# Performance work log

Hardware: AMD Instinct MI355X
Metric: run time of the kernel (lower is better)

The kernel has to match this reference:

```python
import jax, jax.numpy as jnp
import numpy as np

N = 100000   # nodes
E = 800000   # edges
IN = 128     # in_channels == embedding_size (required by residual Linear)
EMB = 128
OUT = 64
EPS = 1e-5   # GraphNorm eps (PyG default)


def setup_inputs() -> dict:
    key = jax.random.key(0)
    ks = jax.random.split(key, 8)
    x = jax.random.normal(ks[0], (N, IN), jnp.float32)
    edge_index = jax.random.randint(ks[1], (2, E), 0, N, dtype=jnp.int64)
    g = lambda k, shape, scale: jax.random.normal(k, shape, jnp.float32) * scale
    return dict(
        x=x,
        edge_index=edge_index,
        W1=g(ks[2], (IN, EMB), IN ** -0.5), b1=jnp.zeros((EMB,), jnp.float32),
        W2=g(ks[3], (EMB, EMB), EMB ** -0.5), b2=jnp.zeros((EMB,), jnp.float32),
        gn1_w=1.0 + g(ks[4], (EMB,), 0.05), gn1_b=jnp.zeros((EMB,), jnp.float32), gn1_ms=jnp.ones((EMB,), jnp.float32),
        gn2_w=1.0 + g(ks[5], (EMB,), 0.05), gn2_b=jnp.zeros((EMB,), jnp.float32), gn2_ms=jnp.ones((EMB,), jnp.float32),
        Wr=g(ks[6], (EMB, OUT), EMB ** -0.5), br=jnp.zeros((OUT,), jnp.float32),
    )


def _gcn_conv(x, W, b, src, dst, dinv):
    # PyG GCNConv: h = x @ W; out[i] = sum_{(j->i)} dinv[j]*dinv[i]*h[j]; out += bias
    h = x @ W
    norm = (dinv[src] * dinv[dst])[:, None]        # [E+N, 1]
    msg = h[src] * norm                             # gather + scale (irregular)
    out = jax.ops.segment_sum(msg, dst, num_segments=N)  # scatter-add
    return out + b


def _graph_norm(h, w, b, ms):
    # PyG GraphNorm, single graph: mean/var over node dim
    mean = jnp.mean(h, axis=0)
    c = h - ms * mean
    var = jnp.mean(c * c, axis=0)
    return w * c * jax.lax.rsqrt(var + EPS) + b


def reference(x, edge_index, W1, b1, W2, b2, gn1_w, gn1_b, gn1_ms, gn2_w, gn2_b, gn2_ms, Wr, br):
    loops = jnp.arange(N, dtype=edge_index.dtype)
    src = jnp.concatenate([edge_index[0], loops])   # add self-loops
    dst = jnp.concatenate([edge_index[1], loops])
    deg = jax.ops.segment_sum(jnp.ones_like(src, dtype=x.dtype), dst, num_segments=N)
    dinv = jnp.where(deg > 0, jax.lax.rsqrt(jnp.maximum(deg, 1.0)), 0.0)

    # dropout is identity in eval mode
    x1 = jax.nn.relu(_graph_norm(_gcn_conv(x, W1, b1, src, dst, dinv), gn1_w, gn1_b, gn1_ms))
    x2 = jax.nn.relu(_graph_norm(_gcn_conv(x1, W2, b2, src, dst, dinv), gn2_w, gn2_b, gn2_ms))
    return (x1 + x2) @ Wr + br
```

## Files before the change

### kernel.cpp

```cpp
#include <hip/hip_runtime.h>
#include <hip/hip_bf16.h>

typedef __attribute__((ext_vector_type(8))) short bf16x8;
typedef __attribute__((ext_vector_type(4))) float f32x4;

#define STATS_BLOCKS 512
#define SLOTS 32

__device__ __forceinline__ float bf2f(unsigned short u){
  union { unsigned int i; float f; } v; v.i = ((unsigned int)u) << 16; return v.f;
}
__device__ __forceinline__ unsigned short f2bf(float f){
  union { float f; unsigned int i; } v; v.f = f;
  return (unsigned short)((v.i + 0x7fffu + ((v.i >> 16) & 1u)) >> 16);
}


__global__ __launch_bounds__(256) void k_zero(int* cur, int N){
  int i = blockIdx.x*256 + threadIdx.x;
  if (i < N) cur[i] = 0;
}

__global__ __launch_bounds__(256) void k_build(const int* __restrict__ src,
    const int* __restrict__ dst, int* cur, int* col, int E){
  int e = blockIdx.x*256 + threadIdx.x;
  if (e >= E) return;
  int d = dst[e];
  int s = src[e];
  int p = atomicAdd(&cur[d], 1);
  if (p < SLOTS) col[d*SLOTS + p] = s;
}

__global__ __launch_bounds__(256) void k_dinv(const int* __restrict__ cur,
                                              float* dinv, int* cnt, int N){
  int i = blockIdx.x*256 + threadIdx.x;
  if (i < N){
    int c = cur[i];
    dinv[i] = rsqrtf((float)(1 + c));
    cnt[i] = min(c, SLOTS);
  }
}


__global__ __launch_bounds__(256) void k_pack(const float* __restrict__ W,
                                              unsigned short* __restrict__ wp, int ncols){
  int idx = blockIdx.x*256 + threadIdx.x;
  if (idx >= 128*ncols) return;
  int b = idx & 7, lane = (idx>>3)&63, kk = (idx>>9)&3, ct = idx>>11;
  int k = kk*32 + ((lane>>4)<<3) + b;
  int c = ct*16 + (lane&15);
  wp[idx] = f2bf(W[k*ncols + c]);
}


__global__ __launch_bounds__(256) void k_gemm1(const float* __restrict__ A,
    const unsigned short* __restrict__ wp, const float* __restrict__ dinv,
    unsigned short* __restrict__ h, int nTiles){
  int gw = (int)((blockIdx.x*256 + threadIdx.x) >> 6);
  if (gw >= nTiles) return;
  int lane = threadIdx.x & 63;
  int row0 = gw*16;
  int r  = row0 + (lane & 15);
  int kb = (lane >> 4) * 8;
  bf16x8 a[4];
#pragma unroll
  for (int kk = 0; kk < 4; ++kk){
    const float* p = A + (size_t)r*128 + kk*32 + kb;
    f32x4 v0 = *reinterpret_cast<const f32x4*>(p);
    f32x4 v1 = *reinterpret_cast<const f32x4*>(p + 4);
#pragma unroll
    for (int b = 0; b < 4; ++b){ a[kk][b] = (short)f2bf(v0[b]); a[kk][4+b] = (short)f2bf(v1[b]); }
  }
  int cst = lane & 15;
  int rb  = row0 + ((lane >> 4) << 2);
  float dv[4];
#pragma unroll
  for (int b2 = 0; b2 < 4; ++b2) dv[b2] = dinv[rb + b2];
#pragma unroll
  for (int ct = 0; ct < 8; ++ct){
    f32x4 acc = {0.f,0.f,0.f,0.f};
#pragma unroll
    for (int kk = 0; kk < 4; ++kk){
      bf16x8 b = *reinterpret_cast<const bf16x8*>(wp + ((ct*4 + kk)*64 + lane)*8);
      acc = __builtin_amdgcn_mfma_f32_16x16x32_bf16(a[kk], b, acc, 0, 0, 0);
    }
    int c = ct*16 + cst;
#pragma unroll
    for (int b2 = 0; b2 < 4; ++b2)
      h[(size_t)(rb + b2)*128 + c] = f2bf(dv[b2]*acc[b2]);
  }
}


__global__ __launch_bounds__(256) void k_agg(const unsigned short* __restrict__ h,
    const float* __restrict__ dinv, const int* __restrict__ cnt,
    const int* __restrict__ col, const float* __restrict__ bias,
    unsigned short* __restrict__ agg, int N){
  int i = (int)((blockIdx.x*256 + threadIdx.x) >> 6);
  if (i >= N) return;
  int lane = threadIdx.x & 63;
  int q  = lane >> 4;
  int cl = lane & 15;
  int c = cnt[i];
  int idx = (lane < c) ? col[i*SLOTS + lane] : i;
  int m16 = (c + 15) & ~15;
  int pads = m16 - c;
  float acc[8];
#pragma unroll
  for (int b = 0; b < 8; ++b) acc[b] = 0.f;
  for (int j = 0; j < m16; j += 16){
    int r0 = __shfl(idx, j + q);
    int r1 = __shfl(idx, j + 4 + q);
    int r2 = __shfl(idx, j + 8 + q);
    int r3 = __shfl(idx, j + 12 + q);
    bf16x8 v0 = *reinterpret_cast<const bf16x8*>(h + (size_t)r0*128 + cl*8);
    bf16x8 v1 = *reinterpret_cast<const bf16x8*>(h + (size_t)r1*128 + cl*8);
    bf16x8 v2 = *reinterpret_cast<const bf16x8*>(h + (size_t)r2*128 + cl*8);
    bf16x8 v3 = *reinterpret_cast<const bf16x8*>(h + (size_t)r3*128 + cl*8);
#pragma unroll
    for (int b = 0; b < 8; ++b)
      acc[b] += (bf2f((unsigned short)v0[b]) + bf2f((unsigned short)v1[b]))
              + (bf2f((unsigned short)v2[b]) + bf2f((unsigned short)v3[b]));
  }
#pragma unroll
  for (int b = 0; b < 8; ++b){
    acc[b] += __shfl_xor(acc[b], 16);
    acc[b] += __shfl_xor(acc[b], 32);
  }
  if (q == 0){
    bf16x8 hs = *reinterpret_cast<const bf16x8*>(h + (size_t)i*128 + cl*8);
    float di = dinv[i];
    float fm = (float)(pads - 1);
    bf16x8 o;
#pragma unroll
    for (int b = 0; b < 8; ++b){
      float s = bf2f((unsigned short)hs[b]);
      float v = di*(acc[b] - fm*s) + bias[cl*8 + b];
      o[b] = (short)f2bf(v);
    }
    *reinterpret_cast<bf16x8*>(agg + (size_t)i*128 + cl*8) = o;
  }
}


__global__ __launch_bounds__(256) void k_stats(const unsigned short* __restrict__ agg,
    float* __restrict__ partials, int N){
  int tid = blockIdx.x*256 + threadIdx.x;
  int g = threadIdx.x & 15;
  int c0 = g * 8;
  float S1[8] = {0,0,0,0,0,0,0,0}, S2[8] = {0,0,0,0,0,0,0,0};
  size_t total = (size_t)N * 16;
  for (size_t p = tid; p < total; p += (size_t)STATS_BLOCKS*256){
    bf16x8 v = reinterpret_cast<const bf16x8*>(agg)[p];
#pragma unroll
    for (int b = 0; b < 8; ++b){
      float f = bf2f((unsigned short)v[b]);
      S1[b] += f; S2[b] += f*f;
    }
  }
  __shared__ float sh1[16][128];
  __shared__ float sh2[16][128];
  int cp = threadIdx.x >> 4;
#pragma unroll
  for (int b = 0; b < 8; ++b){ sh1[cp][c0 + b] = S1[b]; sh2[cp][c0 + b] = S2[b]; }
  __syncthreads();
  int t = threadIdx.x;
  if (t < 128){
    float s = 0.f;
#pragma unroll
    for (int qq = 0; qq < 16; ++qq) s += sh1[qq][t];
    partials[blockIdx.x*256 + t] = s;
  } else {
    int cc = t - 128;
    float s = 0.f;
#pragma unroll
    for (int qq = 0; qq < 16; ++qq) s += sh2[qq][cc];
    partials[blockIdx.x*256 + 128 + cc] = s;
  }
}


__global__ void k_reduce(const float* __restrict__ partials, const float* __restrict__ gw_,
    const float* __restrict__ gb_, const float* __restrict__ gms_,
    float* __restrict__ st, int N){
  int c = threadIdx.x;
  if (c >= 128) return;
  float S1 = 0.f, S2 = 0.f;
  for (int b = 0; b < STATS_BLOCKS; ++b){
    S1 += partials[b*256 + c];
    S2 += partials[b*256 + 128 + c];
  }
  float m  = S1 / (float)N;
  float ms = gms_[c];
  float var = S2/(float)N - 2.f*ms*m*m + ms*ms*m*m;
  float rs = rsqrtf(var + 1e-5f);
  float wv = gw_[c];
  st[c]       = wv * rs;
  st[128 + c] = gb_[c] - wv*rs*ms*m;
}


__global__ __launch_bounds__(256) void k_gemm2(const unsigned short* __restrict__ agg,
    const float* __restrict__ st, const unsigned short* __restrict__ wp,
    const float* __restrict__ dinv, unsigned short* __restrict__ h, int nTiles){
  int gw = (int)((blockIdx.x*256 + threadIdx.x) >> 6);
  if (gw >= nTiles) return;
  int lane = threadIdx.x & 63;
  int row0 = gw*16;
  int r  = row0 + (lane & 15);
  int kb = (lane >> 4) * 8;
  bf16x8 a[4];
#pragma unroll
  for (int kk = 0; kk < 4; ++kk){
    int cb = kk*32 + kb;
    bf16x8 v = *reinterpret_cast<const bf16x8*>(agg + (size_t)r*128 + cb);
    f32x4 s0 = *reinterpret_cast<const f32x4*>(st + cb);
    f32x4 s1 = *reinterpret_cast<const f32x4*>(st + cb + 4);
    f32x4 t0 = *reinterpret_cast<const f32x4*>(st + 128 + cb);
    f32x4 t1 = *reinterpret_cast<const f32x4*>(st + 128 + cb + 4);
#pragma unroll
    for (int b = 0; b < 4; ++b){
      a[kk][b]   = (short)f2bf(fmaxf(0.f, s0[b]*bf2f((unsigned short)v[b])   + t0[b]));
      a[kk][4+b] = (short)f2bf(fmaxf(0.f, s1[b]*bf2f((unsigned short)v[4+b]) + t1[b]));
    }
  }
  int cst = lane & 15;
  int rb  = row0 + ((lane >> 4) << 2);
  float dv[4];
#pragma unroll
  for (int b2 = 0; b2 < 4; ++b2) dv[b2] = dinv[rb + b2];
#pragma unroll
  for (int ct = 0; ct < 8; ++ct){
    f32x4 acc = {0.f,0.f,0.f,0.f};
#pragma unroll
    for (int kk = 0; kk < 4; ++kk){
      bf16x8 b = *reinterpret_cast<const bf16x8*>(wp + ((ct*4 + kk)*64 + lane)*8);
      acc = __builtin_amdgcn_mfma_f32_16x16x32_bf16(a[kk], b, acc, 0, 0, 0);
    }
    int c = ct*16 + cst;
#pragma unroll
    for (int b2 = 0; b2 < 4; ++b2)
      h[(size_t)(rb + b2)*128 + c] = f2bf(dv[b2]*acc[b2]);
  }
}


__global__ __launch_bounds__(256) void k_final(const unsigned short* __restrict__ agg1,
    const unsigned short* __restrict__ agg2, const float* __restrict__ st,
    const unsigned short* __restrict__ wp, const float* __restrict__ br,
    float* __restrict__ out, int nTiles){
  int gw = (int)((blockIdx.x*256 + threadIdx.x) >> 6);
  if (gw >= nTiles) return;
  int lane = threadIdx.x & 63;
  int row0 = gw*16;
  int r  = row0 + (lane & 15);
  int kb = (lane >> 4) * 8;
  bf16x8 a[4];
#pragma unroll
  for (int kk = 0; kk < 4; ++kk){
    int cb = kk*32 + kb;
    bf16x8 g1 = *reinterpret_cast<const bf16x8*>(agg1 + (size_t)r*128 + cb);
    bf16x8 g2 = *reinterpret_cast<const bf16x8*>(agg2 + (size_t)r*128 + cb);
#pragma unroll
    for (int b = 0; b < 8; ++b){
      int c = cb + b;
      float x1v = bf2f(f2bf(fmaxf(0.f, st[c]*bf2f((unsigned short)g1[b]) + st[128 + c])));
      float r2  = fmaxf(0.f, st[256 + c]*bf2f((unsigned short)g2[b]) + st[384 + c]);
      a[kk][b] = (short)f2bf(x1v + r2);
    }
  }
  int cst = lane & 15;
  int rb  = row0 + ((lane >> 4) << 2);
#pragma unroll
  for (int ct = 0; ct < 4; ++ct){
    f32x4 acc = {0.f,0.f,0.f,0.f};
#pragma unroll
    for (int kk = 0; kk < 4; ++kk){
      bf16x8 b = *reinterpret_cast<const bf16x8*>(wp + ((ct*4 + kk)*64 + lane)*8);
      acc = __builtin_amdgcn_mfma_f32_16x16x32_bf16(a[kk], b, acc, 0, 0, 0);
    }
    int c = ct*16 + cst;
    float bias = br[c];
#pragma unroll
    for (int b2 = 0; b2 < 4; ++b2)
      out[(size_t)(rb + b2)*64 + c] = acc[b2] + bias;
  }
}


extern "C" void kernel_launch(void* const* d_in, const int* in_sizes, int n_in,
                              void* d_out, int out_size, void* d_ws, size_t ws_size,
                              hipStream_t stream){
  const float* x    = (const float*)d_in[0];
  const int*   ei   = (const int*)d_in[1];
  const float* W1   = (const float*)d_in[2];
  const float* b1   = (const float*)d_in[3];
  const float* W2   = (const float*)d_in[4];
  const float* b2   = (const float*)d_in[5];
  const float* g1w  = (const float*)d_in[6];
  const float* g1b  = (const float*)d_in[7];
  const float* g1ms = (const float*)d_in[8];
  const float* g2w  = (const float*)d_in[9];
  const float* g2b  = (const float*)d_in[10];
  const float* g2ms = (const float*)d_in[11];
  const float* Wr   = (const float*)d_in[12];
  const float* br   = (const float*)d_in[13];
  float* out = (float*)d_out;

  int N = in_sizes[0] / 128;
  int E = in_sizes[1] / 2;
  const int* srcp = ei;
  const int* dstp = ei + E;

  char* w = (char*)d_ws;
  auto alloc = [&](size_t bytes){ char* p = w; w += (bytes + 255) & ~(size_t)255; return p; };
  float* dinv          = (float*)alloc((size_t)N*4);
  int*   cur           = (int*)  alloc((size_t)N*4);
  int*   cnt           = (int*)  alloc((size_t)N*4);
  int*   col           = (int*)  alloc((size_t)N*SLOTS*4);
  float* partials      = (float*)alloc((size_t)STATS_BLOCKS*256*4);
  float* st            = (float*)alloc(4*128*4);
  unsigned short* wp1  = (unsigned short*)alloc(128*128*2);
  unsigned short* wp2  = (unsigned short*)alloc(128*128*2);
  unsigned short* wpr  = (unsigned short*)alloc(128*64*2);
  unsigned short* h    = (unsigned short*)alloc((size_t)N*128*2);
  unsigned short* agg1 = (unsigned short*)alloc((size_t)N*128*2);
  unsigned short* agg2 = (unsigned short*)alloc((size_t)N*128*2);

  int nTiles = N / 16;
  int gemmBlocks = (nTiles + 3) / 4;
  int nB = (N + 255)/256, eB = (E + 255)/256;
  int aggBlocks = (N*64 + 255)/256;

  k_zero <<<nB, 256, 0, stream>>>(cur, N);
  k_build<<<eB, 256, 0, stream>>>(srcp, dstp, cur, col, E);
  k_dinv <<<nB, 256, 0, stream>>>(cur, dinv, cnt, N);

  k_pack<<<(128*128 + 255)/256, 256, 0, stream>>>(W1, wp1, 128);
  k_pack<<<(128*128 + 255)/256, 256, 0, stream>>>(W2, wp2, 128);
  k_pack<<<(128*64  + 255)/256, 256, 0, stream>>>(Wr, wpr, 64);

  k_gemm1<<<gemmBlocks, 256, 0, stream>>>(x, wp1, dinv, h, nTiles);
  k_agg  <<<aggBlocks, 256, 0, stream>>>(h, dinv, cnt, col, b1, agg1, N);
  k_stats<<<STATS_BLOCKS, 256, 0, stream>>>(agg1, partials, N);
  k_reduce<<<1, 128, 0, stream>>>(partials, g1w, g1b, g1ms, st, N);

  k_gemm2<<<gemmBlocks, 256, 0, stream>>>(agg1, st, wp2, dinv, h, nTiles);
  k_agg  <<<aggBlocks, 256, 0, stream>>>(h, dinv, cnt, col, b2, agg2, N);
  k_stats<<<STATS_BLOCKS, 256, 0, stream>>>(agg2, partials, N);
  k_reduce<<<1, 128, 0, stream>>>(partials, g2w, g2b, g2ms, st + 256, N);

  k_final<<<gemmBlocks, 256, 0, stream>>>(agg1, agg2, st, wpr, br, out, nTiles);
}
```

Measured before the change: 244.8 us.

## Fuse setup kernels, drop dinv buffer, partition edge build, shrink agg padding

Merges the zero-fill and weight-pack kernels into one launch and removes the dinv kernel by computing rsqrt(1+deg) inline from the counts. The CSR build is partitioned so each block handles one eighth of destination nodes, to localise atomics, at the cost of reading dst eight times. Aggregation now pads neighbour lists to multiples of 8 instead of 16, cutting wasted gathers. The stats reduction uses half as many partial blocks and all 256 threads.

```diff
diff --git a/kernel.cpp b/kernel.cpp
--- a/kernel.cpp
+++ b/kernel.cpp
@@ -4,7 +4,7 @@
 typedef __attribute__((ext_vector_type(8))) short bf16x8;
 typedef __attribute__((ext_vector_type(4))) float f32x4;
 
-#define STATS_BLOCKS 512
+#define STATS_BLOCKS 256
 #define SLOTS 32
 
 __device__ __forceinline__ float bf2f(unsigned short u){
@@ -16,45 +16,52 @@
 }
 
 
-__global__ __launch_bounds__(256) void k_zero(int* cur, int N){
-  int i = blockIdx.x*256 + threadIdx.x;
-  if (i < N) cur[i] = 0;
-}
-
-__global__ __launch_bounds__(256) void k_build(const int* __restrict__ src,
-    const int* __restrict__ dst, int* cur, int* col, int E){
-  int e = blockIdx.x*256 + threadIdx.x;
-  if (e >= E) return;
-  int d = dst[e];
-  int s = src[e];
-  int p = atomicAdd(&cur[d], 1);
-  if (p < SLOTS) col[d*SLOTS + p] = s;
-}
-
-__global__ __launch_bounds__(256) void k_dinv(const int* __restrict__ cur,
-                                              float* dinv, int* cnt, int N){
-  int i = blockIdx.x*256 + threadIdx.x;
-  if (i < N){
-    int c = cur[i];
-    dinv[i] = rsqrtf((float)(1 + c));
-    cnt[i] = min(c, SLOTS);
-  }
-}
-
-
-__global__ __launch_bounds__(256) void k_pack(const float* __restrict__ W,
-                                              unsigned short* __restrict__ wp, int ncols){
-  int idx = blockIdx.x*256 + threadIdx.x;
+__global__ __launch_bounds__(256) void k_setup(int* cur, int N,
+    const float* __restrict__ W1, const float* __restrict__ W2, const float* __restrict__ Wr,
+    unsigned short* __restrict__ wp1, unsigned short* __restrict__ wp2,
+    unsigned short* __restrict__ wpr){
+  int nB = (N + 255) >> 8;
+  int b = blockIdx.x;
+  if (b < nB){
+    int i = b*256 + threadIdx.x;
+    if (i < N) cur[i] = 0;
+    return;
+  }
+  int pb = b - nB;
+  const float* W; unsigned short* wp; int ncols;
+  if (pb < 64)      { W = W1; wp = wp1; ncols = 128; }
+  else if (pb < 128){ W = W2; wp = wp2; ncols = 128; pb -= 64; }
+  else              { W = Wr; wp = wpr; ncols = 64;  pb -= 128; }
+  int idx = pb*256 + threadIdx.x;
   if (idx >= 128*ncols) return;
-  int b = idx & 7, lane = (idx>>3)&63, kk = (idx>>9)&3, ct = idx>>11;
-  int k = kk*32 + ((lane>>4)<<3) + b;
+  int bb = idx & 7, lane = (idx>>3)&63, kk = (idx>>9)&3, ct = idx>>11;
+  int k = kk*32 + ((lane>>4)<<3) + bb;
   int c = ct*16 + (lane&15);
   wp[idx] = f2bf(W[k*ncols + c]);
 }
 
 
+__global__ __launch_bounds__(256) void k_build(const int* __restrict__ src,
+    const int* __restrict__ dst, int* cur, int* col, int E, int N8){
+  int r = blockIdx.x & 7;
+  int chunk = blockIdx.x >> 3;
+  int nchunks = gridDim.x >> 3;
+  int per = (E + nchunks - 1) / nchunks;
+  int e0 = chunk * per;
+  int e1 = min(E, e0 + per);
+  int lo = r * N8, hi = lo + N8;
+  for (int e = e0 + threadIdx.x; e < e1; e += 256){
+    int d = dst[e];
+    if (d >= lo && d < hi){
+      int p = atomicAdd(&cur[d], 1);
+      if (p < SLOTS) col[d*SLOTS + p] = src[e];
+    }
+  }
+}
+
+
 __global__ __launch_bounds__(256) void k_gemm1(const float* __restrict__ A,
-    const unsigned short* __restrict__ wp, const float* __restrict__ dinv,
+    const unsigned short* __restrict__ wp, const int* __restrict__ cur,
     unsigned short* __restrict__ h, int nTiles){
   int gw = (int)((blockIdx.x*256 + threadIdx.x) >> 6);
   if (gw >= nTiles) return;
@@ -75,7 +82,7 @@
   int rb  = row0 + ((lane >> 4) << 2);
   float dv[4];
 #pragma unroll
-  for (int b2 = 0; b2 < 4; ++b2) dv[b2] = dinv[rb + b2];
+  for (int b2 = 0; b2 < 4; ++b2) dv[b2] = rsqrtf(1.0f + (float)cur[rb + b2]);
 #pragma unroll
   for (int ct = 0; ct < 8; ++ct){
     f32x4 acc = {0.f,0.f,0.f,0.f};
@@ -93,34 +100,29 @@
 
 
 __global__ __launch_bounds__(256) void k_agg(const unsigned short* __restrict__ h,
-    const float* __restrict__ dinv, const int* __restrict__ cnt,
-    const int* __restrict__ col, const float* __restrict__ bias,
-    unsigned short* __restrict__ agg, int N){
+    const int* __restrict__ cur, const int* __restrict__ col,
+    const float* __restrict__ bias, unsigned short* __restrict__ agg, int N){
   int i = (int)((blockIdx.x*256 + threadIdx.x) >> 6);
   if (i >= N) return;
   int lane = threadIdx.x & 63;
   int q  = lane >> 4;
   int cl = lane & 15;
-  int c = cnt[i];
+  int craw = cur[i];
+  int c = min(craw, SLOTS);
   int idx = (lane < c) ? col[i*SLOTS + lane] : i;
-  int m16 = (c + 15) & ~15;
-  int pads = m16 - c;
+  int m8 = (c + 7) & ~7;
+  int pads = m8 - c;
   float acc[8];
 #pragma unroll
   for (int b = 0; b < 8; ++b) acc[b] = 0.f;
-  for (int j = 0; j < m16; j += 16){
+  for (int j = 0; j < m8; j += 8){
     int r0 = __shfl(idx, j + q);
     int r1 = __shfl(idx, j + 4 + q);
-    int r2 = __shfl(idx, j + 8 + q);
-    int r3 = __shfl(idx, j + 12 + q);
     bf16x8 v0 = *reinterpret_cast<const bf16x8*>(h + (size_t)r0*128 + cl*8);
     bf16x8 v1 = *reinterpret_cast<const bf16x8*>(h + (size_t)r1*128 + cl*8);
-    bf16x8 v2 = *reinterpret_cast<const bf16x8*>(h + (size_t)r2*128 + cl*8);
-    bf16x8 v3 = *reinterpret_cast<const bf16x8*>(h + (size_t)r3*128 + cl*8);
 #pragma unroll
     for (int b = 0; b < 8; ++b)
-      acc[b] += (bf2f((unsigned short)v0[b]) + bf2f((unsigned short)v1[b]))
-              + (bf2f((unsigned short)v2[b]) + bf2f((unsigned short)v3[b]));
+      acc[b] += bf2f((unsigned short)v0[b]) + bf2f((unsigned short)v1[b]);
   }
 #pragma unroll
   for (int b = 0; b < 8; ++b){
@@ -129,7 +131,7 @@
   }
   if (q == 0){
     bf16x8 hs = *reinterpret_cast<const bf16x8*>(h + (size_t)i*128 + cl*8);
-    float di = dinv[i];
+    float di = rsqrtf(1.0f + (float)craw);
     float fm = (float)(pads - 1);
     bf16x8 o;
 #pragma unroll
@@ -183,13 +185,17 @@
 __global__ void k_reduce(const float* __restrict__ partials, const float* __restrict__ gw_,
     const float* __restrict__ gb_, const float* __restrict__ gms_,
     float* __restrict__ st, int N){
-  int c = threadIdx.x;
-  if (c >= 128) return;
-  float S1 = 0.f, S2 = 0.f;
-  for (int b = 0; b < STATS_BLOCKS; ++b){
-    S1 += partials[b*256 + c];
-    S2 += partials[b*256 + 128 + c];
-  }
+  int t = threadIdx.x;
+  float S = 0.f;
+#pragma unroll 8
+  for (int b = 0; b < STATS_BLOCKS; ++b)
+    S += partials[b*256 + t];
+  __shared__ float sh[256];
+  sh[t] = S;
+  __syncthreads();
+  if (t >= 128) return;
+  int c = t;
+  float S1 = sh[c], S2 = sh[128 + c];
   float m  = S1 / (float)N;
   float ms = gms_[c];
   float var = S2/(float)N - 2.f*ms*m*m + ms*ms*m*m;
@@ -202,7 +208,7 @@
 
 __global__ __launch_bounds__(256) void k_gemm2(const unsigned short* __restrict__ agg,
     const float* __restrict__ st, const unsigned short* __restrict__ wp,
-    const float* __restrict__ dinv, unsigned short* __restrict__ h, int nTiles){
+    const int* __restrict__ cur, unsigned short* __restrict__ h, int nTiles){
   int gw = (int)((blockIdx.x*256 + threadIdx.x) >> 6);
   if (gw >= nTiles) return;
   int lane = threadIdx.x & 63;
@@ -228,7 +234,7 @@
   int rb  = row0 + ((lane >> 4) << 2);
   float dv[4];
 #pragma unroll
-  for (int b2 = 0; b2 < 4; ++b2) dv[b2] = dinv[rb + b2];
+  for (int b2 = 0; b2 < 4; ++b2) dv[b2] = rsqrtf(1.0f + (float)cur[rb + b2]);
 #pragma unroll
   for (int ct = 0; ct < 8; ++ct){
     f32x4 acc = {0.f,0.f,0.f,0.f};
@@ -314,9 +320,7 @@
 
   char* w = (char*)d_ws;
   auto alloc = [&](size_t bytes){ char* p = w; w += (bytes + 255) & ~(size_t)255; return p; };
-  float* dinv          = (float*)alloc((size_t)N*4);
   int*   cur           = (int*)  alloc((size_t)N*4);
-  int*   cnt           = (int*)  alloc((size_t)N*4);
   int*   col           = (int*)  alloc((size_t)N*SLOTS*4);
   float* partials      = (float*)alloc((size_t)STATS_BLOCKS*256*4);
   float* st            = (float*)alloc(4*128*4);
@@ -329,26 +333,23 @@
 
   int nTiles = N / 16;
   int gemmBlocks = (nTiles + 3) / 4;
-  int nB = (N + 255)/256, eB = (E + 255)/256;
+  int nB = (N + 255)/256;
+  int N8 = (N + 7) / 8;
+  int buildBlocks = 8 * 256;
   int aggBlocks = (N*64 + 255)/256;
 
-  k_zero <<<nB, 256, 0, stream>>>(cur, N);
-  k_build<<<eB, 256, 0, stream>>>(srcp, dstp, cur, col, E);
-  k_dinv <<<nB, 256, 0, stream>>>(cur, dinv, cnt, N);
-
-  k_pack<<<(128*128 + 255)/256, 256, 0, stream>>>(W1, wp1, 128);
-  k_pack<<<(128*128 + 255)/256, 256, 0, stream>>>(W2, wp2, 128);
-  k_pack<<<(128*64  + 255)/256, 256, 0, stream>>>(Wr, wpr, 64);
-
-  k_gemm1<<<gemmBlocks, 256, 0, stream>>>(x, wp1, dinv, h, nTiles);
-  k_agg  <<<aggBlocks, 256, 0, stream>>>(h, dinv, cnt, col, b1, agg1, N);
+  k_setup<<<nB + 160, 256, 0, stream>>>(cur, N, W1, W2, Wr, wp1, wp2, wpr);
+  k_build<<<buildBlocks, 256, 0, stream>>>(srcp, dstp, cur, col, E, N8);
+
+  k_gemm1<<<gemmBlocks, 256, 0, stream>>>(x, wp1, cur, h, nTiles);
+  k_agg  <<<aggBlocks, 256, 0, stream>>>(h, cur, col, b1, agg1, N);
   k_stats<<<STATS_BLOCKS, 256, 0, stream>>>(agg1, partials, N);
-  k_reduce<<<1, 128, 0, stream>>>(partials, g1w, g1b, g1ms, st, N);
-
-  k_gemm2<<<gemmBlocks, 256, 0, stream>>>(agg1, st, wp2, dinv, h, nTiles);
-  k_agg  <<<aggBlocks, 256, 0, stream>>>(h, dinv, cnt, col, b2, agg2, N);
+  k_reduce<<<1, 256, 0, stream>>>(partials, g1w, g1b, g1ms, st, N);
+
+  k_gemm2<<<gemmBlocks, 256, 0, stream>>>(agg1, st, wp2, cur, h, nTiles);
+  k_agg  <<<aggBlocks, 256, 0, stream>>>(h, cur, col, b2, agg2, N);
   k_stats<<<STATS_BLOCKS, 256, 0, stream>>>(agg2, partials, N);
-  k_reduce<<<1, 128, 0, stream>>>(partials, g2w, g2b, g2ms, st + 256, N);
+  k_reduce<<<1, 256, 0, stream>>>(partials, g2w, g2b, g2ms, st + 256, N);
 
   k_final<<<gemmBlocks, 256, 0, stream>>>(agg1, agg2, st, wpr, br, out, nTiles);
 }
```

New measurement: 230.0 us. -6.0%, faster.
